# Performance work log

Measured on AMD Instinct MI355X. Metric: run time of the kernel, lower is better.

Reference implementation:

```python
import jax, jax.numpy as jnp
import numpy as np

V, E_DIM, HID, GNN_O, HEADS = 50257, 256, 128, 128, 4
N_NODES, N_EDGES, T_LEN = 10000, 160000, 64
NEG_SLOPE = 0.2


def gatv2(x, src, dst, Wl, Wr, att, bias, concat):
    """PyG GATv2Conv (share_weights=False, self-loops already in src/dst)."""
    heads, out_ch = att.shape
    n = x.shape[0]
    xl = (x @ Wl).reshape(n, heads, out_ch)   # source transform
    xr = (x @ Wr).reshape(n, heads, out_ch)   # target transform
    e = jax.nn.leaky_relu(xl[src] + xr[dst], NEG_SLOPE)        # [E, h, c]
    logits = jnp.einsum('ehc,hc->eh', e, att)                  # [E, h]
    m = jax.ops.segment_max(logits, dst, num_segments=n)
    a = jnp.exp(logits - m[dst])
    a = a / jax.ops.segment_sum(a, dst, num_segments=n)[dst]
    out = jax.ops.segment_sum(xl[src] * a[..., None], dst, num_segments=n)
    out = out.reshape(n, heads * out_ch) if concat else out.mean(axis=1)
    return out + bias


def setup_inputs() -> dict:
    key = jax.random.key(0)
    ks = jax.random.split(key, 16)
    g = lambda k, shape: jax.random.normal(k, shape, jnp.float32) * 0.05
    x_nodes = jax.random.randint(ks[0], (N_NODES,), 0, V)
    edge_index = jax.random.randint(ks[1], (2, N_EDGES), 0, N_NODES)
    target_sequence = jax.random.randint(ks[2], (1, T_LEN), 0, V)
    return dict(
        x_nodes=x_nodes, edge_index=edge_index, target_sequence=target_sequence,
        embedding=g(ks[3], (V, E_DIM)),
        W1l=g(ks[4], (E_DIM, HEADS * HID)), W1r=g(ks[5], (E_DIM, HEADS * HID)),
        att1=g(ks[6], (HEADS, HID)), b1=jnp.zeros((HEADS * HID,), jnp.float32),
        W2l=g(ks[7], (HEADS * HID, GNN_O)), W2r=g(ks[8], (HEADS * HID, GNN_O)),
        att2=g(ks[9], (1, GNN_O)), b2=jnp.zeros((GNN_O,), jnp.float32),
        Wih=g(ks[10], (3 * HID, GNN_O + E_DIM)), Whh=g(ks[11], (3 * HID, HID)),
        bih=jnp.zeros((3 * HID,), jnp.float32), bhh=jnp.zeros((3 * HID,), jnp.float32),
        Wout=g(ks[12], (V, HID)), bout=jnp.zeros((V,), jnp.float32),
    )


def reference(x_nodes, edge_index, target_sequence, embedding,
              W1l, W1r, att1, b1, W2l, W2r, att2, b2,
              Wih, Whh, bih, bhh, Wout, bout):
    n = x_nodes.shape[0]
    loops = jnp.arange(n, dtype=edge_index.dtype)
    src = jnp.concatenate([edge_index[0], loops])   # add self-loops (PyG default)
    dst = jnp.concatenate([edge_index[1], loops])
    feats = embedding[x_nodes]                      # [N, E_DIM] (dropout off: eval)
    h1 = jax.nn.elu(gatv2(feats, src, dst, W1l, W1r, att1, b1, concat=True))
    enc = gatv2(h1, src, dst, W2l, W2r, att2, b2, concat=False)  # [N, GNN_O]
    context = enc.mean(axis=0)                      # constant across decode steps

    # teacher forcing (ratio=1.0): input tokens are SOS(0) then shifted targets
    tokens = jnp.concatenate([jnp.zeros((1,), target_sequence.dtype),
                              target_sequence[0, :-1]])

    def step(h, tok):
        x = jnp.concatenate([embedding[tok], context])          # [E_DIM+GNN_O]
        gi = Wih @ x + bih
        gh = Whh @ h + bhh
        ir, iz, inn = jnp.split(gi, 3)
        hr, hz, hn = jnp.split(gh, 3)
        r = jax.nn.sigmoid(ir + hr)
        z = jax.nn.sigmoid(iz + hz)
        cand = jnp.tanh(inn + r * hn)
        h_new = (1.0 - z) * cand + z * h
        logits = Wout @ h_new + bout
        return h_new, logits

    h0 = jnp.zeros((Whh.shape[1],), jnp.float32)
    _, logits = jax.lax.scan(step, h0, tokens)      # [T, V]
    return logits[None]                              # [1, T, V]
```

## Files before the change

### kernel.cpp

```cpp
#include <hip/hip_runtime.h>
#include <hip/hip_bf16.h>
#include <math.h>

#define NNODES 10000
#define NEDGES 160000
#define EDIM   256
#define HIDC   128
#define TLEN   64
#define VOCAB  50257
#define NEG    0.2f

typedef __bf16 bf16x8 __attribute__((ext_vector_type(8)));
typedef float  f32x4  __attribute__((ext_vector_type(4)));

static __device__ __forceinline__ float leaky(float x){ return x > 0.f ? x : NEG*x; }
static __device__ __forceinline__ float sigm (float x){ return __fdividef(1.f, 1.f + __expf(-x)); }
static __device__ __forceinline__ float eluf (float x){ return x > 0.f ? x : expm1f(x); }
static __device__ __forceinline__ unsigned short bf16rn(float f){
  unsigned a = __float_as_uint(f);
  return (unsigned short)((a + 0x7FFFu + ((a >> 16) & 1u)) >> 16);
}
static __device__ __forceinline__ float upf(unsigned short u){ return __uint_as_float(((unsigned)u) << 16); }

#define PB_FEATS 2500
#define PB_WCAST 8783
#define PB_TR1L  8815
#define PB_TR1R  8847
#define PB_TR2L  8863
#define PB_TR2R  8879
#define PB_ZERO  8919

static __device__ void tr_dev(const float* __restrict__ in, unsigned short* __restrict__ out,
                              int K, int Nin, int bx, int by, int t,
                              unsigned short (*tile)[72])
{
  int k0 = bx*64, n0 = by*64;
  int tr = t >> 4, tc4 = (t & 15)*4;
  #pragma unroll
  for (int it = 0; it < 4; ++it){
    int kr = tr + 16*it;
    float4 v = *(const float4*)(in + (size_t)(k0+kr)*Nin + n0 + tc4);
    tile[tc4+0][kr] = bf16rn(v.x);
    tile[tc4+1][kr] = bf16rn(v.y);
    tile[tc4+2][kr] = bf16rn(v.z);
    tile[tc4+3][kr] = bf16rn(v.w);
  }
  __syncthreads();
  #pragma unroll
  for (int it = 0; it < 4; ++it){
    int nr = tr + 16*it;
    ushort4 o;
    o.x = tile[nr][tc4+0]; o.y = tile[nr][tc4+1];
    o.z = tile[nr][tc4+2]; o.w = tile[nr][tc4+3];
    *(ushort4*)(out + (size_t)(n0+nr)*K + k0 + tc4) = o;
  }
}

__global__ __launch_bounds__(256) void k_prep(
    const int* __restrict__ xn, const float* __restrict__ emb,
    unsigned short* __restrict__ featsb,
    const float* __restrict__ Wout, unsigned short* __restrict__ Woutb,
    const float* __restrict__ W1l, const float* __restrict__ W1r, unsigned short* __restrict__ Bt1,
    const float* __restrict__ W2l, const float* __restrict__ W2r, unsigned short* __restrict__ Bt2,
    int* __restrict__ deg, int* __restrict__ cursor, float* __restrict__ ctx)
{
  __shared__ unsigned short tile[64][72];
  int b = blockIdx.x, t = threadIdx.x;
  if (b < PB_FEATS){
    int node = b*4 + (t >> 6);
    int l = t & 63;
    float4 v = ((const float4*)(emb + (size_t)xn[node]*EDIM))[l];
    ushort4 o; o.x = bf16rn(v.x); o.y = bf16rn(v.y); o.z = bf16rn(v.z); o.w = bf16rn(v.w);
    *(ushort4*)(featsb + (size_t)node*EDIM + 4*l) = o;
  } else if (b < PB_WCAST){
    int idx = (b - PB_FEATS)*256 + t;
    if (idx < VOCAB*HIDC/4){
      float4 v = ((const float4*)Wout)[idx];
      ushort4 o; o.x = bf16rn(v.x); o.y = bf16rn(v.y); o.z = bf16rn(v.z); o.w = bf16rn(v.w);
      ((ushort4*)Woutb)[idx] = o;
    }
  } else if (b < PB_TR1L){
    int lb = b - PB_WCAST;  tr_dev(W1l, Bt1,           256, 512, lb & 3, lb >> 2, t, tile);
  } else if (b < PB_TR1R){
    int lb = b - PB_TR1L;   tr_dev(W1r, Bt1 + 512*256, 256, 512, lb & 3, lb >> 2, t, tile);
  } else if (b < PB_TR2L){
    int lb = b - PB_TR1R;   tr_dev(W2l, Bt2,           512, 128, lb & 7, lb >> 3, t, tile);
  } else if (b < PB_TR2R){
    int lb = b - PB_TR2L;   tr_dev(W2r, Bt2 + 128*512, 512, 128, lb & 7, lb >> 3, t, tile);
  } else {
    int gid = (b - PB_TR2R)*256 + t;
    if (gid < NNODES){ deg[gid] = 0; cursor[gid] = 0; }
    if (gid < HIDC) ctx[gid] = 0.f;
  }
}

__global__ void k_deg(const int* __restrict__ dst, int* __restrict__ deg){
  int e = blockIdx.x*256 + threadIdx.x;
  if (e < NEDGES) atomicAdd(&deg[dst[e]], 1);
}

__global__ __launch_bounds__(1024) void k_scan(const int* __restrict__ deg, int* __restrict__ offs){
  __shared__ int s[1024];
  int t = threadIdx.x;
  int loc[10]; int sum = 0;
  #pragma unroll
  for (int q = 0; q < 10; q++){
    int idx = t*10 + q;
    loc[q] = sum;
    sum += (idx < NNODES) ? deg[idx] : 0;
  }
  s[t] = sum;
  __syncthreads();
  for (int ofs = 1; ofs < 1024; ofs <<= 1){
    int v = (t >= ofs) ? s[t-ofs] : 0;
    __syncthreads();
    s[t] += v;
    __syncthreads();
  }
  int pre = (t > 0) ? s[t-1] : 0;
  #pragma unroll
  for (int q = 0; q < 10; q++){
    int idx = t*10 + q;
    if (idx < NNODES) offs[idx] = pre + loc[q];
  }
  if (t == 1023) offs[NNODES] = s[1023];
}

__global__ void k_scatter(const int* __restrict__ src, const int* __restrict__ dst,
                          const int* __restrict__ offs, int* __restrict__ cursor,
                          int* __restrict__ esrc){
  int e = blockIdx.x*256 + threadIdx.x;
  if (e >= NEDGES) return;
  int d = dst[e];
  int p = atomicAdd(&cursor[d], 1);
  esrc[offs[d] + p] = src[e];
}

template<int KDIM>
__global__ __launch_bounds__(256) void k_mfma(const unsigned short* __restrict__ A,
    const unsigned short* __restrict__ Bt, unsigned short* __restrict__ C,
    int M, int N)
{
  __shared__ __align__(16) unsigned short As[128*64];
  __shared__ __align__(16) unsigned short Bs[128*64];
  int tid = threadIdx.x;
  int l   = tid & 63;
  int wid = tid >> 6;
  int wr = wid >> 1, wc = wid & 1;
  int row0 = blockIdx.x * 128, col0 = blockIdx.y * 128;
  int lr = l & 15, kg = l >> 4;
  f32x4 acc[4][4] = {};

  for (int kt = 0; kt < KDIM/64; ++kt){
    int k0 = kt*64;
    #pragma unroll
    for (int c = 0; c < 4; ++c){
      int chunk = wid*4 + c;
      int arow = row0 + chunk*8 + (l >> 3);
      if (arow > M-1) arow = M-1;
      const unsigned short* ga = A + (size_t)arow*KDIM + k0 + (l & 7)*8;
      __builtin_amdgcn_global_load_lds(
          (const __attribute__((address_space(1))) void*)ga,
          (__attribute__((address_space(3))) void*)(As + chunk*512), 16, 0, 0);
      int brow = col0 + chunk*8 + (l >> 3);
      const unsigned short* gb = Bt + (size_t)brow*KDIM + k0 + (l & 7)*8;
      __builtin_amdgcn_global_load_lds(
          (const __attribute__((address_space(1))) void*)gb,
          (__attribute__((address_space(3))) void*)(Bs + chunk*512), 16, 0, 0);
    }
    __syncthreads();
    #pragma unroll
    for (int ks = 0; ks < 2; ++ks){
      bf16x8 af[4], bfr[4];
      #pragma unroll
      for (int m = 0; m < 4; ++m)
        af[m] = *(const bf16x8*)(As + (wr*64 + m*16 + lr)*64 + ks*32 + kg*8);
      #pragma unroll
      for (int n = 0; n < 4; ++n)
        bfr[n] = *(const bf16x8*)(Bs + (wc*64 + n*16 + lr)*64 + ks*32 + kg*8);
      #pragma unroll
      for (int m = 0; m < 4; ++m)
        #pragma unroll
        for (int n = 0; n < 4; ++n)
          acc[m][n] = __builtin_amdgcn_mfma_f32_16x16x32_bf16(af[m], bfr[n], acc[m][n], 0, 0, 0);
    }
    __syncthreads();
  }

  #pragma unroll
  for (int m = 0; m < 4; ++m){
    int rbase = row0 + wr*64 + m*16 + kg*4;
    #pragma unroll
    for (int r = 0; r < 4; ++r){
      int row = rbase + r;
      if (row < M){
        #pragma unroll
        for (int n = 0; n < 4; ++n){
          int col = col0 + wc*64 + n*16 + lr;
          C[(size_t)row*N + col] = bf16rn(acc[m][n][r]);
        }
      }
    }
  }
}

__global__ __launch_bounds__(256) void k_mout(const unsigned short* __restrict__ A,
    const unsigned short* __restrict__ Bt, const float* __restrict__ bias,
    float* __restrict__ out)
{
  __shared__ __align__(16) unsigned short As[64*128];
  __shared__ __align__(16) unsigned short Bs[128*128];
  int tid = threadIdx.x;
  int l   = tid & 63;
  int wid = tid >> 6;
  int col0 = blockIdx.x * 128;
  int lr = l & 15, kg = l >> 4;

  #pragma unroll
  for (int c = 0; c < 4; ++c){
    int chunk = wid*4 + c;
    const unsigned short* ga = A + (size_t)(chunk*4 + (l >> 4))*128 + (l & 15)*8;
    __builtin_amdgcn_global_load_lds(
        (const __attribute__((address_space(1))) void*)ga,
        (__attribute__((address_space(3))) void*)(As + chunk*512), 16, 0, 0);
  }
  #pragma unroll
  for (int c = 0; c < 8; ++c){
    int chunk = wid*8 + c;
    int brow = col0 + chunk*4 + (l >> 4);
    if (brow > VOCAB-1) brow = VOCAB-1;
    const unsigned short* gb = Bt + (size_t)brow*128 + (l & 15)*8;
    __builtin_amdgcn_global_load_lds(
        (const __attribute__((address_space(1))) void*)gb,
        (__attribute__((address_space(3))) void*)(Bs + chunk*512), 16, 0, 0);
  }
  __syncthreads();

  f32x4 acc[4][2] = {};
  #pragma unroll
  for (int ks = 0; ks < 4; ++ks){
    bf16x8 af[4], bfr[2];
    #pragma unroll
    for (int m = 0; m < 4; ++m)
      af[m] = *(const bf16x8*)(As + (m*16 + lr)*128 + ks*32 + kg*8);
    #pragma unroll
    for (int n = 0; n < 2; ++n)
      bfr[n] = *(const bf16x8*)(Bs + (wid*32 + n*16 + lr)*128 + ks*32 + kg*8);
    #pragma unroll
    for (int m = 0; m < 4; ++m)
      #pragma unroll
      for (int n = 0; n < 2; ++n)
        acc[m][n] = __builtin_amdgcn_mfma_f32_16x16x32_bf16(af[m], bfr[n], acc[m][n], 0, 0, 0);
  }

  #pragma unroll
  for (int n = 0; n < 2; ++n){
    int col = col0 + wid*32 + n*16 + lr;
    if (col < VOCAB){
      float bv = bias[col];
      #pragma unroll
      for (int m = 0; m < 4; ++m){
        #pragma unroll
        for (int r = 0; r < 4; ++r){
          int trow = m*16 + kg*4 + r;
          out[(size_t)trow*VOCAB + col] = acc[m][n][r] + bv;
        }
      }
    }
  }
}

__global__ __launch_bounds__(256) void k_gat1(const unsigned short* __restrict__ xlr,
    const int* __restrict__ esrc, const int* __restrict__ offs,
    const float* __restrict__ att, const float* __restrict__ b1,
    unsigned short* __restrict__ h1b)
{
  int node = blockIdx.x*4 + (threadIdx.x >> 6);
  int l = threadIdx.x & 63;
  const unsigned short* bi = xlr + (size_t)node*1024;
  ushort4 u;
  u = *(const ushort4*)(bi + 512 + 4*l);
  float4 xr1; xr1.x = upf(u.x); xr1.y = upf(u.y); xr1.z = upf(u.z); xr1.w = upf(u.w);
  u = *(const ushort4*)(bi + 768 + 4*l);
  float4 xr2; xr2.x = upf(u.x); xr2.y = upf(u.y); xr2.z = upf(u.z); xr2.w = upf(u.w);
  int hq = l >> 5;
  float4 at1 = *(const float4*)(att + hq*HIDC + ((4*l) & 127));
  float4 at2 = *(const float4*)(att + (2+hq)*HIDC + ((4*l) & 127));
  float4 ac1 = {0,0,0,0}, ac2 = {0,0,0,0};
  float d1 = 0.f, d2 = 0.f;
  int beg = offs[node], end = offs[node+1];
  for (int p = beg-1; p < end; ++p){
    int s = (p < beg) ? node : esrc[p];
    const unsigned short* bs = xlr + (size_t)s*1024;
    ushort4 u1 = *(const ushort4*)(bs + 4*l);
    ushort4 u2 = *(const ushort4*)(bs + 256 + 4*l);
    float4 x1; x1.x = upf(u1.x); x1.y = upf(u1.y); x1.z = upf(u1.z); x1.w = upf(u1.w);
    float4 x2; x2.x = upf(u2.x); x2.y = upf(u2.y); x2.z = upf(u2.z); x2.w = upf(u2.w);
    float p1 = leaky(x1.x+xr1.x)*at1.x + leaky(x1.y+xr1.y)*at1.y
             + leaky(x1.z+xr1.z)*at1.z + leaky(x1.w+xr1.w)*at1.w;
    float p2 = leaky(x2.x+xr2.x)*at2.x + leaky(x2.y+xr2.y)*at2.y
             + leaky(x2.z+xr2.z)*at2.z + leaky(x2.w+xr2.w)*at2.w;
    #pragma unroll
    for (int m = 1; m <= 16; m <<= 1){
      p1 += __shfl_xor(p1, m);
      p2 += __shfl_xor(p2, m);
    }
    float w1 = __expf(p1), w2 = __expf(p2);
    ac1.x = fmaf(w1, x1.x, ac1.x); ac1.y = fmaf(w1, x1.y, ac1.y);
    ac1.z = fmaf(w1, x1.z, ac1.z); ac1.w = fmaf(w1, x1.w, ac1.w);
    ac2.x = fmaf(w2, x2.x, ac2.x); ac2.y = fmaf(w2, x2.y, ac2.y);
    ac2.z = fmaf(w2, x2.z, ac2.z); ac2.w = fmaf(w2, x2.w, ac2.w);
    d1 += w1; d2 += w2;
  }
  float i1 = 1.f/d1, i2 = 1.f/d2;
  const float* bq1 = b1 + 4*l;
  const float* bq2 = b1 + 256 + 4*l;
  ushort4 o1, o2;
  o1.x = bf16rn(eluf(ac1.x*i1 + bq1[0])); o1.y = bf16rn(eluf(ac1.y*i1 + bq1[1]));
  o1.z = bf16rn(eluf(ac1.z*i1 + bq1[2])); o1.w = bf16rn(eluf(ac1.w*i1 + bq1[3]));
  o2.x = bf16rn(eluf(ac2.x*i2 + bq2[0])); o2.y = bf16rn(eluf(ac2.y*i2 + bq2[1]));
  o2.z = bf16rn(eluf(ac2.z*i2 + bq2[2])); o2.w = bf16rn(eluf(ac2.w*i2 + bq2[3]));
  *(ushort4*)(h1b + (size_t)node*512 + 4*l)       = o1;
  *(ushort4*)(h1b + (size_t)node*512 + 256 + 4*l) = o2;
}

__global__ __launch_bounds__(256) void k_gat2(const unsigned short* __restrict__ xlr2,
    const int* __restrict__ esrc, const int* __restrict__ offs,
    const float* __restrict__ att2, const float* __restrict__ b2,
    float* __restrict__ enc)
{
  int node = blockIdx.x*4 + (threadIdx.x >> 6);
  int l = threadIdx.x & 63;
  const unsigned short* bi = xlr2 + (size_t)node*256;
  ushort2 v = *(const ushort2*)(bi + 128 + 2*l);
  float2 xr; xr.x = upf(v.x); xr.y = upf(v.y);
  float2 at = *(const float2*)(att2 + 2*l);
  float2 ac = {0,0}; float den = 0.f;
  int beg = offs[node], end = offs[node+1];
  for (int p = beg-1; p < end; ++p){
    int s = (p < beg) ? node : esrc[p];
    ushort2 xv = *(const ushort2*)(xlr2 + (size_t)s*256 + 2*l);
    float2 x; x.x = upf(xv.x); x.y = upf(xv.y);
    float pp = leaky(x.x+xr.x)*at.x + leaky(x.y+xr.y)*at.y;
    #pragma unroll
    for (int m = 1; m <= 32; m <<= 1) pp += __shfl_xor(pp, m);
    float w = __expf(pp);
    ac.x = fmaf(w, x.x, ac.x); ac.y = fmaf(w, x.y, ac.y);
    den += w;
  }
  float inv = 1.f/den;
  float2 o; o.x = ac.x*inv + b2[2*l]; o.y = ac.y*inv + b2[2*l+1];
  *(float2*)(enc + (size_t)node*128 + 2*l) = o;
}

__global__ void k_mean(const float* __restrict__ enc, float* __restrict__ ctx){
  int c = threadIdx.x & 127;
  int slice = blockIdx.x*2 + (threadIdx.x >> 7);
  float s = 0.f;
  for (int i = slice; i < NNODES; i += 160) s += enc[(size_t)i*128 + c];
  atomicAdd(&ctx[c], s * (1.f/NNODES));
}

__global__ __launch_bounds__(384) void k_gi(const int* __restrict__ tseq,
    const float* __restrict__ emb, const float* __restrict__ ctx,
    const float* __restrict__ Wih, const float* __restrict__ bih,
    float* __restrict__ Gi)
{
  __shared__ float xs[384];
  int t = blockIdx.x, tid = threadIdx.x;
  int tok = (t == 0) ? 0 : tseq[t-1];
  if (tid < 256) xs[tid] = emb[(size_t)tok*EDIM + tid];
  else           xs[tid] = ctx[tid - 256];
  __syncthreads();
  const float* w = Wih + (size_t)tid*384;
  float acc = bih[tid];
  #pragma unroll 8
  for (int k = 0; k < 384; k++) acc = fmaf(w[k], xs[k], acc);
  Gi[t*384 + tid] = acc;
}

__global__ __launch_bounds__(384) void k_gru(const float* __restrict__ Gi,
    const float* __restrict__ Whh, const float* __restrict__ bhh,
    unsigned short* __restrict__ HTt)
{
  __shared__ float GH[384];
  __shared__ alignas(16) float HS[128];
  int tid = threadIdx.x;
  float w[128];
  {
    const float4* wrow = (const float4*)(Whh + (size_t)tid*HIDC);
    #pragma unroll
    for (int k = 0; k < 32; k++){
      float4 v = wrow[k];
      w[4*k+0] = v.x; w[4*k+1] = v.y; w[4*k+2] = v.z; w[4*k+3] = v.w;
    }
  }
  float bh = bhh[tid];
  float hloc = 0.f;
  if (tid < 128) HS[tid] = 0.f;
  __syncthreads();

  const float4* H4 = (const float4*)HS;

  for (int t = 0; t < TLEN; t++){
    float gi0 = 0.f, gi1 = 0.f, gi2 = 0.f;
    if (tid < 128){
      gi0 = Gi[t*384 + tid];
      gi1 = Gi[t*384 + 128 + tid];
      gi2 = Gi[t*384 + 256 + tid];
    }
    float a0 = 0.f, a1 = 0.f, a2 = 0.f, a3 = 0.f;
    #pragma unroll
    for (int q = 0; q < 16; q++){
      float4 ha = H4[2*q];
      float4 hb = H4[2*q+1];
      a0 = fmaf(w[8*q+0], ha.x, a0);
      a1 = fmaf(w[8*q+1], ha.y, a1);
      a2 = fmaf(w[8*q+2], ha.z, a2);
      a3 = fmaf(w[8*q+3], ha.w, a3);
      a0 = fmaf(w[8*q+4], hb.x, a0);
      a1 = fmaf(w[8*q+5], hb.y, a1);
      a2 = fmaf(w[8*q+6], hb.z, a2);
      a3 = fmaf(w[8*q+7], hb.w, a3);
    }
    float acc = ((a0 + a1) + (a2 + a3)) + bh;
    if (tid >= 128) GH[tid] = acc;
    __syncthreads();
    if (tid < 128){
      float gr = gi0 + acc;
      float gz = gi1 + GH[128 + tid];
      float hn = GH[256 + tid];
      float r = sigm(gr);
      float z = sigm(gz);
      float e2 = __expf(2.f*(gi2 + r*hn));
      float cand = __fdividef(e2 - 1.f, e2 + 1.f);
      float hnew = (1.f - z)*cand + z*hloc;
      hloc = hnew;
      HS[tid] = hnew;
      HTt[t*HIDC + tid] = bf16rn(hnew);
    }
    __syncthreads();
  }
}

extern "C" void kernel_launch(void* const* d_in, const int* in_sizes, int n_in,
                              void* d_out, int out_size, void* d_ws, size_t ws_size,
                              hipStream_t stream)
{
  const int*   x_nodes = (const int*)  d_in[0];
  const int*   eidx    = (const int*)  d_in[1];
  const int*   tseq    = (const int*)  d_in[2];
  const float* emb     = (const float*)d_in[3];
  const float* W1l     = (const float*)d_in[4];
  const float* W1r     = (const float*)d_in[5];
  const float* att1    = (const float*)d_in[6];
  const float* b1      = (const float*)d_in[7];
  const float* W2l     = (const float*)d_in[8];
  const float* W2r     = (const float*)d_in[9];
  const float* att2    = (const float*)d_in[10];
  const float* b2      = (const float*)d_in[11];
  const float* Wih     = (const float*)d_in[12];
  const float* Whh     = (const float*)d_in[13];
  const float* bih     = (const float*)d_in[14];
  const float* bhh     = (const float*)d_in[15];
  const float* Wout    = (const float*)d_in[16];
  const float* bout    = (const float*)d_in[17];
  float* out = (float*)d_out;
  char*  ws  = (char*)d_ws;

  unsigned short* xlr1b  = (unsigned short*)(ws);
  unsigned short* h1b    = (unsigned short*)(ws + 20480000);
  unsigned short* featsb = (unsigned short*)(ws + 30720000);
  unsigned short* xlr2b  = (unsigned short*)(ws + 35840000);
  float*          enc    = (float*)        (ws + 40960000);
  unsigned short* Bt1    = (unsigned short*)(ws + 46080000);
  unsigned short* Bt2    = (unsigned short*)(ws + 46604288);
  int*   deg    = (int*)(ws + 46866432);
  int*   offs   = (int*)(ws + 46906432);
  int*   cursor = (int*)(ws + 46946436);
  int*   esrc   = (int*)(ws + 46986436);
  float* ctx    = (float*)(ws + 47626440);
  float* Gi     = (float*)(ws + 47627008);
  unsigned short* HTt   = (unsigned short*)(ws + 47725312);
  unsigned short* Woutb = (unsigned short*)(ws + 47741696);

  k_prep<<<PB_ZERO, 256, 0, stream>>>(x_nodes, emb, featsb, Wout, Woutb,
                                      W1l, W1r, Bt1, W2l, W2r, Bt2,
                                      deg, cursor, ctx);

  k_deg    <<<625, 256, 0, stream>>>(eidx + NEDGES, deg);
  k_scan   <<<1,  1024, 0, stream>>>(deg, offs);
  k_scatter<<<625, 256, 0, stream>>>(eidx, eidx + NEDGES, offs, cursor, esrc);

  k_mfma<256><<<dim3(79,8), 256, 0, stream>>>(featsb, Bt1, xlr1b, NNODES, 1024);
  k_gat1<<<2500, 256, 0, stream>>>(xlr1b, esrc, offs, att1, b1, h1b);

  k_mfma<512><<<dim3(79,2), 256, 0, stream>>>(h1b, Bt2, xlr2b, NNODES, 256);
  k_gat2<<<2500, 256, 0, stream>>>(xlr2b, esrc, offs, att2, b2, enc);

  k_mean<<<80, 256, 0, stream>>>(enc, ctx);
  k_gi  <<<TLEN, 384, 0, stream>>>(tseq, emb, ctx, Wih, bih, Gi);
  k_gru <<<1, 384, 0, stream>>>(Gi, Whh, bhh, HTt);

  k_mout<<<393, 256, 0, stream>>>(HTt, Woutb, bout, out);
}
```

Measured before the change: 259.6 us.

## Fuse context mean into GAT2 and split GRU input projection by linearity

The node-wise mean of the GAT2 output is now accumulated inside k_gat2 through shared-memory and global atomics, so the enc buffer and the k_mean kernel are no longer needed. The GRU input projection is split into an embedding part and a context part. The embedding part is computed early in extra k_prep blocks, and the context part is a single matvec done once at the start of k_gru, with bias b2 folded in there. This removes the separate k_gi launch and its dependence on ctx, taking two launches off the serial tail. The cost is heavy atomic contention on ctx, 2500 blocks times 128 atomics, and a nondeterministic float summation order.

```diff
diff --git a/kernel.cpp b/kernel.cpp
--- a/kernel.cpp
+++ b/kernel.cpp
@@ -29,6 +29,7 @@
 #define PB_TR2L  8863
 #define PB_TR2R  8879
 #define PB_ZERO  8919
+#define PB_AT    9047
 
 static __device__ void tr_dev(const float* __restrict__ in, unsigned short* __restrict__ out,
                               int K, int Nin, int bx, int by, int t,
@@ -62,9 +63,12 @@
     const float* __restrict__ Wout, unsigned short* __restrict__ Woutb,
     const float* __restrict__ W1l, const float* __restrict__ W1r, unsigned short* __restrict__ Bt1,
     const float* __restrict__ W2l, const float* __restrict__ W2r, unsigned short* __restrict__ Bt2,
-    int* __restrict__ deg, int* __restrict__ cursor, float* __restrict__ ctx)
+    int* __restrict__ deg, int* __restrict__ cursor, float* __restrict__ ctx,
+    const int* __restrict__ tseq, const float* __restrict__ Wih,
+    const float* __restrict__ bih, float* __restrict__ At)
 {
   __shared__ unsigned short tile[64][72];
+  __shared__ __align__(16) float xe[EDIM];
   int b = blockIdx.x, t = threadIdx.x;
   if (b < PB_FEATS){
     int node = b*4 + (t >> 6);
@@ -87,10 +91,31 @@
     int lb = b - PB_TR1R;   tr_dev(W2l, Bt2,           512, 128, lb & 7, lb >> 3, t, tile);
   } else if (b < PB_TR2R){
     int lb = b - PB_TR2L;   tr_dev(W2r, Bt2 + 128*512, 512, 128, lb & 7, lb >> 3, t, tile);
-  } else {
+  } else if (b < PB_ZERO){
     int gid = (b - PB_TR2R)*256 + t;
     if (gid < NNODES){ deg[gid] = 0; cursor[gid] = 0; }
     if (gid < HIDC) ctx[gid] = 0.f;
+  } else {
+    int lb = b - PB_ZERO;
+    int tt = lb >> 1;
+    int row = (lb & 1)*192 + t;
+    int tok = (tt == 0) ? 0 : tseq[tt-1];
+    {
+      if (t < 64) ((float4*)xe)[t] = ((const float4*)(emb + (size_t)tok*EDIM))[t];
+      __syncthreads();
+    }
+    if (t < 192){
+      const float4* w4 = (const float4*)(Wih + (size_t)row*384);
+      const float4* x4 = (const float4*)xe;
+      float a0 = 0.f, a1 = 0.f, a2 = 0.f, a3 = 0.f;
+      #pragma unroll
+      for (int k = 0; k < 64; k++){
+        float4 w = w4[k]; float4 x = x4[k];
+        a0 = fmaf(w.x, x.x, a0); a1 = fmaf(w.y, x.y, a1);
+        a2 = fmaf(w.z, x.z, a2); a3 = fmaf(w.w, x.w, a3);
+      }
+      At[tt*384 + row] = ((a0 + a1) + (a2 + a3)) + bih[row];
+    }
   }
 }
 
@@ -326,11 +351,13 @@
 
 __global__ __launch_bounds__(256) void k_gat2(const unsigned short* __restrict__ xlr2,
     const int* __restrict__ esrc, const int* __restrict__ offs,
-    const float* __restrict__ att2, const float* __restrict__ b2,
-    float* __restrict__ enc)
-{
+    const float* __restrict__ att2, float* __restrict__ ctx)
+{
+  __shared__ float csum[128];
   int node = blockIdx.x*4 + (threadIdx.x >> 6);
   int l = threadIdx.x & 63;
+  if (threadIdx.x < 128) csum[threadIdx.x] = 0.f;
+  __syncthreads();
   const unsigned short* bi = xlr2 + (size_t)node*256;
   ushort2 v = *(const ushort2*)(bi + 128 + 2*l);
   float2 xr; xr.x = upf(v.x); xr.y = upf(v.y);
@@ -349,42 +376,23 @@
     den += w;
   }
   float inv = 1.f/den;
-  float2 o; o.x = ac.x*inv + b2[2*l]; o.y = ac.y*inv + b2[2*l+1];
-  *(float2*)(enc + (size_t)node*128 + 2*l) = o;
-}
-
-__global__ void k_mean(const float* __restrict__ enc, float* __restrict__ ctx){
-  int c = threadIdx.x & 127;
-  int slice = blockIdx.x*2 + (threadIdx.x >> 7);
-  float s = 0.f;
-  for (int i = slice; i < NNODES; i += 160) s += enc[(size_t)i*128 + c];
-  atomicAdd(&ctx[c], s * (1.f/NNODES));
-}
-
-__global__ __launch_bounds__(384) void k_gi(const int* __restrict__ tseq,
-    const float* __restrict__ emb, const float* __restrict__ ctx,
-    const float* __restrict__ Wih, const float* __restrict__ bih,
-    float* __restrict__ Gi)
-{
-  __shared__ float xs[384];
-  int t = blockIdx.x, tid = threadIdx.x;
-  int tok = (t == 0) ? 0 : tseq[t-1];
-  if (tid < 256) xs[tid] = emb[(size_t)tok*EDIM + tid];
-  else           xs[tid] = ctx[tid - 256];
-  __syncthreads();
-  const float* w = Wih + (size_t)tid*384;
-  float acc = bih[tid];
-  #pragma unroll 8
-  for (int k = 0; k < 384; k++) acc = fmaf(w[k], xs[k], acc);
-  Gi[t*384 + tid] = acc;
-}
-
-__global__ __launch_bounds__(384) void k_gru(const float* __restrict__ Gi,
+  atomicAdd(&csum[2*l],   ac.x*inv);
+  atomicAdd(&csum[2*l+1], ac.y*inv);
+  __syncthreads();
+  if (threadIdx.x < 128)
+    atomicAdd(&ctx[threadIdx.x], csum[threadIdx.x] * (1.f/NNODES));
+}
+
+__global__ __launch_bounds__(384) void k_gru(const float* __restrict__ At,
+    const float* __restrict__ ctx, const float* __restrict__ b2,
+    const float* __restrict__ Wih,
     const float* __restrict__ Whh, const float* __restrict__ bhh,
     unsigned short* __restrict__ HTt)
 {
   __shared__ float GH[384];
   __shared__ alignas(16) float HS[128];
+  __shared__ alignas(16) float CTX[128];
+  __shared__ float CROW[384];
   int tid = threadIdx.x;
   float w[128];
   {
@@ -397,7 +405,23 @@
   }
   float bh = bhh[tid];
   float hloc = 0.f;
-  if (tid < 128) HS[tid] = 0.f;
+  if (tid < 128){ HS[tid] = 0.f; CTX[tid] = ctx[tid] + b2[tid]; }
+  __syncthreads();
+  {
+    const float4* wi = (const float4*)(Wih + (size_t)tid*384 + 256);
+    const float4* c4 = (const float4*)CTX;
+    float a0 = 0.f, a1 = 0.f, a2 = 0.f, a3 = 0.f;
+    #pragma unroll
+    for (int k = 0; k < 32; k++){
+      float4 ww = wi[k]; float4 cc = c4[k];
+      a0 = fmaf(ww.x, cc.x, a0); a1 = fmaf(ww.y, cc.y, a1);
+      a2 = fmaf(ww.z, cc.z, a2); a3 = fmaf(ww.w, cc.w, a3);
+    }
+    CROW[tid] = ((a0 + a1) + (a2 + a3));
+  }
+  __syncthreads();
+  float c0 = 0.f, c1 = 0.f, c2 = 0.f;
+  if (tid < 128){ c0 = CROW[tid]; c1 = CROW[128 + tid]; c2 = CROW[256 + tid]; }
   __syncthreads();
 
   const float4* H4 = (const float4*)HS;
@@ -405,9 +429,9 @@
   for (int t = 0; t < TLEN; t++){
     float gi0 = 0.f, gi1 = 0.f, gi2 = 0.f;
     if (tid < 128){
-      gi0 = Gi[t*384 + tid];
-      gi1 = Gi[t*384 + 128 + tid];
-      gi2 = Gi[t*384 + 256 + tid];
+      gi0 = At[t*384 + tid]       + c0;
+      gi1 = At[t*384 + 128 + tid] + c1;
+      gi2 = At[t*384 + 256 + tid] + c2;
     }
     float a0 = 0.f, a1 = 0.f, a2 = 0.f, a3 = 0.f;
     #pragma unroll
@@ -472,7 +496,6 @@
   unsigned short* h1b    = (unsigned short*)(ws + 20480000);
   unsigned short* featsb = (unsigned short*)(ws + 30720000);
   unsigned short* xlr2b  = (unsigned short*)(ws + 35840000);
-  float*          enc    = (float*)        (ws + 40960000);
   unsigned short* Bt1    = (unsigned short*)(ws + 46080000);
   unsigned short* Bt2    = (unsigned short*)(ws + 46604288);
   int*   deg    = (int*)(ws + 46866432);
@@ -480,13 +503,13 @@
   int*   cursor = (int*)(ws + 46946436);
   int*   esrc   = (int*)(ws + 46986436);
   float* ctx    = (float*)(ws + 47626440);
-  float* Gi     = (float*)(ws + 47627008);
+  float* At     = (float*)(ws + 47627008);
   unsigned short* HTt   = (unsigned short*)(ws + 47725312);
   unsigned short* Woutb = (unsigned short*)(ws + 47741696);
 
-  k_prep<<<PB_ZERO, 256, 0, stream>>>(x_nodes, emb, featsb, Wout, Woutb,
-                                      W1l, W1r, Bt1, W2l, W2r, Bt2,
-                                      deg, cursor, ctx);
+  k_prep<<<PB_AT, 256, 0, stream>>>(x_nodes, emb, featsb, Wout, Woutb,
+                                    W1l, W1r, Bt1, W2l, W2r, Bt2,
+                                    deg, cursor, ctx, tseq, Wih, bih, At);
 
   k_deg    <<<625, 256, 0, stream>>>(eidx + NEDGES, deg);
   k_scan   <<<1,  1024, 0, stream>>>(deg, offs);
@@ -496,11 +519,9 @@
   k_gat1<<<2500, 256, 0, stream>>>(xlr1b, esrc, offs, att1, b1, h1b);
 
   k_mfma<512><<<dim3(79,2), 256, 0, stream>>>(h1b, Bt2, xlr2b, NNODES, 256);
-  k_gat2<<<2500, 256, 0, stream>>>(xlr2b, esrc, offs, att2, b2, enc);
-
-  k_mean<<<80, 256, 0, stream>>>(enc, ctx);
-  k_gi  <<<TLEN, 384, 0, stream>>>(tseq, emb, ctx, Wih, bih, Gi);
-  k_gru <<<1, 384, 0, stream>>>(Gi, Whh, bhh, HTt);
+  k_gat2<<<2500, 256, 0, stream>>>(xlr2b, esrc, offs, att2, ctx);
+
+  k_gru <<<1, 384, 0, stream>>>(At, ctx, b2, Wih, Whh, bhh, HTt);
 
   k_mout<<<393, 256, 0, stream>>>(HTt, Woutb, bout, out);
 }
```

Measured after the change: 323.3 us. 24.5% more time.
